# Kernel tuning notes

Hardware: AMD Instinct MI355X
Metric: run time of the kernel (lower is better)

The kernel has to match this reference:

```python
import jax, jax.numpy as jnp
import numpy as np

NUM_HEADS = 16
NEG_INF = -1e30  # finite large negative; avoids NaN on fully-masked padded query rows


def setup_inputs() -> dict:
    key = jax.random.key(0)
    k0, k1, k2, k3 = jax.random.split(key, 4)
    B, S, E = 4, 2048, 1024
    x_padded = jax.random.normal(k0, (B, S, E), dtype=jnp.float32)
    # variable lengths in [S//2, S] so no batch row is fully empty
    seq_lengths = jax.random.randint(k1, (B,), S // 2, S + 1).astype(jnp.int32)
    Wqkv = jax.random.normal(k2, (3 * E, E), dtype=jnp.float32) * 0.02  # torch Linear weight [out,in]
    Wout = jax.random.normal(k3, (E, E), dtype=jnp.float32) * 0.02
    return {"x_padded": x_padded, "Wqkv": Wqkv, "Wout": Wout,
            "seq_lengths": seq_lengths, "window_left": 512, "window_right": 0}


def _build_mask(seq_lengths, S, window_left, window_right):
    # key-side padding mask: [B, S]
    pad = jnp.arange(S)[None, :] < seq_lengths[:, None]
    mask = pad[:, None, None, :]  # [B,1,1,S]
    if window_left >= 0 or window_right >= 0:
        i = jnp.arange(S)[:, None]
        j = jnp.arange(S)[None, :]
        win = jnp.ones((S, S), dtype=bool)
        if window_left >= 0:
            win = win & (j >= i - window_left)
        if window_right >= 0:
            win = win & (j <= i + window_right)
        mask = mask & win[None, None, :, :]
    elif (window_left, window_right) == (-1, 0):
        causal = jnp.tril(jnp.ones((S, S), dtype=bool))
        mask = mask & causal[None, None, :, :]
    return mask  # [B,1,S,S] (broadcasts over heads)


def reference(x_padded, Wqkv, Wout, seq_lengths, window_left, window_right):
    B, S, E = x_padded.shape
    H = NUM_HEADS
    D = E // H
    scale = 1.0 / jnp.sqrt(jnp.float32(D))
    qkv = x_padded @ Wqkv.T  # [B,S,3E]
    q, k, v = jnp.split(qkv, 3, axis=-1)
    q = q.reshape(B, S, H, D).transpose(0, 2, 1, 3)  # [B,H,S,D]
    k = k.reshape(B, S, H, D).transpose(0, 2, 1, 3)
    v = v.reshape(B, S, H, D).transpose(0, 2, 1, 3)
    mask = _build_mask(seq_lengths, S, window_left, window_right)
    scores = jnp.einsum("bhid,bhjd->bhij", q, k) * scale
    scores = jnp.where(mask, scores, NEG_INF)
    attn = jax.nn.softmax(scores, axis=-1)
    out = jnp.einsum("bhij,bhjd->bhid", attn, v)  # [B,H,S,D]
    out = out.transpose(0, 2, 1, 3).reshape(B, S, E)
    return out @ Wout.T
```

## Files before the change

### kernel.cpp

```cpp
#include <hip/hip_runtime.h>

typedef __bf16 bf16;
typedef __attribute__((ext_vector_type(2))) __bf16 bf16x2;
typedef __attribute__((ext_vector_type(4))) __bf16 bf16x4;
typedef __attribute__((ext_vector_type(8))) __bf16 bf16x8;
typedef __attribute__((ext_vector_type(4))) float f32x4;
typedef __attribute__((ext_vector_type(16))) float f32x16;

#define B_ 4
#define S_ 2048
#define H_ 16
#define D_ 64
#define E_ 1024

#define BM 256
#define BN 128
#define BK 64

__device__ __forceinline__ int imin(int a, int b) { return a < b ? a : b; }
__device__ __forceinline__ int imax(int a, int b) { return a > b ? a : b; }

__device__ __forceinline__ void gload_lds16(const void* g, void* l) {
  __builtin_amdgcn_global_load_lds(
      (const __attribute__((address_space(1))) void*)g,
      (__attribute__((address_space(3))) void*)l, 16, 0, 0);
}

__global__ __launch_bounds__(256) void cvt3_kernel(
    const float* __restrict__ x, bf16* __restrict__ xb,
    const float* __restrict__ wqkv, bf16* __restrict__ wqkvb,
    const float* __restrict__ wout, bf16* __restrict__ woutb) {
  const int bid = blockIdx.x;
  const float* in;
  bf16* out;
  int idx;
  if (bid < 4096) { in = x; out = xb; idx = bid; }
  else if (bid < 5632) { in = wqkv; out = wqkvb; idx = bid - 4096; }
  else { in = wout; out = woutb; idx = bid - 5632; }
  const int i = (idx * 256 + threadIdx.x) * 8;
  float4 v0 = *(const float4*)(in + i);
  float4 v1 = *(const float4*)(in + i + 4);
  bf16x8 o;
  o[0] = (bf16)v0.x; o[1] = (bf16)v0.y; o[2] = (bf16)v0.z; o[3] = (bf16)v0.w;
  o[4] = (bf16)v1.x; o[5] = (bf16)v1.y; o[6] = (bf16)v1.z; o[7] = (bf16)v1.w;
  *(bf16x8*)(out + i) = o;
}

__global__ __launch_bounds__(512, 1) void gemm_pipe(
    const bf16* __restrict__ A, const bf16* __restrict__ Bm,
    int M, int N, int K, int mode,
    bf16* __restrict__ qd, bf16* __restrict__ kd, bf16* __restrict__ vtd,
    float* __restrict__ outf) {
  __shared__ __align__(16) bf16 As[3][BM * BK];
  __shared__ __align__(16) bf16 Bs[3][BN * BK];
  const int tid = threadIdx.x;
  const int wave = tid >> 6, lane = tid & 63;
  const int l15 = lane & 15, l4 = lane >> 4;
  const int wm = (wave >> 1) * 64;
  const int wn = (wave & 1) * 64;

  const int nwg = gridDim.x * gridDim.y;
  const int fid = blockIdx.y * gridDim.x + blockIdx.x;
  const int chunk = nwg >> 3;
  const int swz = (fid & 7) * chunk + (fid >> 3);
  const int tn = swz % gridDim.x;
  const int tm = swz / gridDim.x;

  const bf16* Abase = A + (size_t)tm * BM * K;
  const bf16* Bbase = Bm + (size_t)tn * BN * K;

  f32x4 acc[4][4];
#pragma unroll
  for (int i = 0; i < 4; ++i)
#pragma unroll
    for (int j = 0; j < 4; ++j)
#pragma unroll
      for (int r = 0; r < 4; ++r) acc[i][j][r] = 0.f;

  const int NT = K >> 6;

#define STAGE_A(sbuf, k0)                                                      \
  {                                                                            \
    _Pragma("unroll") for (int ld = 0; ld < 4; ++ld) {                         \
      const int idx = ld * 512 + tid;                                          \
      const int row = idx >> 3, g = idx & 7;                                   \
      const int gs = g ^ (row & 7);                                            \
      gload_lds16(Abase + (size_t)row * K + (k0) + gs * 8,                     \
                  As[sbuf] + (ld * 512 + wave * 64) * 8);                      \
    }                                                                          \
  }
#define STAGE_B(sbuf, k0)                                                      \
  {                                                                            \
    _Pragma("unroll") for (int ld = 0; ld < 2; ++ld) {                         \
      const int idx = ld * 512 + tid;                                          \
      const int row = idx >> 3, g = idx & 7;                                   \
      const int gs = g ^ (row & 7);                                            \
      gload_lds16(Bbase + (size_t)row * K + (k0) + gs * 8,                     \
                  Bs[sbuf] + (ld * 512 + wave * 64) * 8);                      \
    }                                                                          \
  }

  STAGE_A(0, 0); STAGE_B(0, 0);
  STAGE_A(1, BK); STAGE_B(1, BK);
  asm volatile("s_waitcnt vmcnt(6)" ::: "memory");
  __builtin_amdgcn_s_barrier();

  int p = 0;
  for (int t = 0; t < NT; ++t) {
    const bf16* Ap = As[p];
    const bf16* Bp = Bs[p];
    const int sb = (p + 2 >= 3) ? p - 1 : p + 2;
    const int sk0 = ((t + 2 < NT) ? t + 2 : NT - 1) * BK;

    bf16x8 a[4], bfr[4];
#pragma unroll
    for (int i = 0; i < 4; ++i) {
      const int ra = wm + i * 16 + l15;
      a[i] = *(const bf16x8*)(Ap + ra * 64 + ((l4 ^ (ra & 7)) * 8));
      const int rb = wn + i * 16 + l15;
      bfr[i] = *(const bf16x8*)(Bp + rb * 64 + ((l4 ^ (rb & 7)) * 8));
    }
    STAGE_A(sb, sk0);
    __builtin_amdgcn_s_barrier();
    asm volatile("s_waitcnt lgkmcnt(0)" ::: "memory");
    __builtin_amdgcn_sched_barrier(0);
    __builtin_amdgcn_s_setprio(1);
#pragma unroll
    for (int i = 0; i < 4; ++i)
#pragma unroll
      for (int j = 0; j < 4; ++j)
        acc[i][j] = __builtin_amdgcn_mfma_f32_16x16x32_bf16(a[i], bfr[j],
                                                            acc[i][j], 0, 0, 0);
    __builtin_amdgcn_s_setprio(0);
    __builtin_amdgcn_s_barrier();

#pragma unroll
    for (int i = 0; i < 4; ++i) {
      const int ra = wm + i * 16 + l15;
      a[i] = *(const bf16x8*)(Ap + ra * 64 + (((4 + l4) ^ (ra & 7)) * 8));
      const int rb = wn + i * 16 + l15;
      bfr[i] = *(const bf16x8*)(Bp + rb * 64 + (((4 + l4) ^ (rb & 7)) * 8));
    }
    STAGE_B(sb, sk0);
    __builtin_amdgcn_s_barrier();
    asm volatile("s_waitcnt lgkmcnt(0)" ::: "memory");
    __builtin_amdgcn_sched_barrier(0);
    __builtin_amdgcn_s_setprio(1);
#pragma unroll
    for (int i = 0; i < 4; ++i)
#pragma unroll
      for (int j = 0; j < 4; ++j)
        acc[i][j] = __builtin_amdgcn_mfma_f32_16x16x32_bf16(a[i], bfr[j],
                                                            acc[i][j], 0, 0, 0);
    __builtin_amdgcn_s_setprio(0);

    asm volatile("s_waitcnt vmcnt(6)" ::: "memory");
    __builtin_amdgcn_s_barrier();
    p = (p + 1 >= 3) ? 0 : p + 1;
  }
#undef STAGE_A
#undef STAGE_B

  if (mode == 0) {
#pragma unroll
    for (int i = 0; i < 4; ++i) {
      const int m0 = tm * BM + wm + i * 16 + l4 * 4;
      const int b = m0 >> 11, s = m0 & (S_ - 1);
#pragma unroll
      for (int j = 0; j < 4; ++j) {
        const int n = tn * BN + wn + j * 16 + l15;
        const int which = n >> 10;
        const int hn = n & 1023;
        const int h = hn >> 6, d = hn & 63;
        const f32x4 av = acc[i][j];
        if (which == 0) {
#pragma unroll
          for (int r = 0; r < 4; ++r)
            qd[((size_t)(b * H_ + h) * S_ + (s + r)) * D_ + d] =
                (bf16)(av[r] * 0.125f);
        } else if (which == 1) {
#pragma unroll
          for (int r = 0; r < 4; ++r)
            kd[((size_t)(b * H_ + h) * S_ + (s + r)) * D_ + d] = (bf16)av[r];
        } else {
          bf16x4 pv;
#pragma unroll
          for (int r = 0; r < 4; ++r) pv[r] = (bf16)av[r];
          *(bf16x4*)(vtd + ((size_t)(b * H_ + h) * D_ + d) * S_ + s) = pv;
        }
      }
    }
  } else {
#pragma unroll
    for (int i = 0; i < 4; ++i) {
      const int m0 = tm * BM + wm + i * 16 + l4 * 4;
#pragma unroll
      for (int j = 0; j < 4; ++j) {
        const int n = tn * BN + wn + j * 16 + l15;
#pragma unroll
        for (int r = 0; r < 4; ++r) outf[(size_t)(m0 + r) * N + n] = acc[i][j][r];
      }
    }
  }
}

__global__ __launch_bounds__(256) void meanv_kernel(const bf16* __restrict__ vt,
                                                    float* __restrict__ meanv) {
  const int bh = blockIdx.x >> 2, dq = blockIdx.x & 3;
  const int tid = threadIdx.x;
  const int dl = tid >> 4;
  const int sl = tid & 15;
  const int d = dq * 16 + dl;
  const bf16* row = vt + ((size_t)bh * D_ + d) * S_;
  float s = 0.f;
#pragma unroll
  for (int it = 0; it < 16; ++it) {
    bf16x8 v = *(const bf16x8*)(row + it * 128 + sl * 8);
#pragma unroll
    for (int j = 0; j < 8; ++j) s += (float)v[j];
  }
#pragma unroll
  for (int m = 1; m < 16; m <<= 1) s += __shfl_xor(s, m, 64);
  if (sl == 0) meanv[(size_t)bh * D_ + d] = s * (1.0f / (float)S_);
}

__device__ __forceinline__ int pk2(float a, float b) {
  union { bf16x2 h; int i; } u;
  u.h[0] = (bf16)a; u.h[1] = (bf16)b;
  return u.i;
}

__global__ __launch_bounds__(256) void attn_kernel(
    const bf16* __restrict__ q, const bf16* __restrict__ k,
    const bf16* __restrict__ vt, const float* __restrict__ meanv,
    const int* __restrict__ seq_lengths, const int* __restrict__ wlp,
    const int* __restrict__ wrp, bf16* __restrict__ attn_out) {
  __shared__ __align__(16) bf16 Ks[2][64 * 64];
  __shared__ __align__(16) bf16 Vs[2][64 * 64];
  const int tid = threadIdx.x, wave = tid >> 6, lane = tid & 63;
  const int l31 = lane & 31, l5 = lane >> 5;
  const int bid0 = blockIdx.x;
  const int bid = (bid0 & 7) * 128 + (bid0 >> 3);
  const int bh = bid >> 4;
  const int g = bid & 15;
  const int b = bh >> 4, h = bh & 15;
  const int q0b = g * 128;
  const int q0w = q0b + wave * 32;
  const int seq_len = seq_lengths[b];
  const int wl = wlp[0], wr = wrp[0];

  const bf16* qbase = q + (size_t)bh * S_ * D_;
  const bf16* kbase = k + (size_t)bh * S_ * D_;
  const bf16* vtb = vt + (size_t)bh * D_ * S_;

  bf16x8 qa[4];
#pragma unroll
  for (int dg = 0; dg < 4; ++dg)
    qa[dg] = *(const bf16x8*)(qbase + (size_t)(q0w + l31) * D_ + dg * 16 + l5 * 8);

  const int hi_blk = (wr >= 0) ? imin(q0b + 127 + wr, S_ - 1) : (S_ - 1);
  const int end_blk = imin(hi_blk + 1, seq_len);
  const int lo_blk = (wl >= 0) ? imax(0, q0b - wl) : 0;
  const int beg_blk = lo_blk & ~63;
  const int ntb = (end_blk > beg_blk) ? ((end_blk - beg_blk + 63) >> 6) : 0;

  const int w_hi = (wr >= 0) ? (q0w + 31 + wr) : (S_ - 1);
  const int w_end = imin(w_hi + 1, seq_len);
  const int w_lo = (wl >= 0) ? imax(0, q0w - wl) : 0;

  f32x16 o0, o1;
#pragma unroll
  for (int r = 0; r < 16; ++r) { o0[r] = 0.f; o1[r] = 0.f; }
  float mrun = -1e30f, lrun = 0.f;

#define STAGE(bufb, kt0)                                                       \
  {                                                                            \
    _Pragma("unroll") for (int ld = 0; ld < 2; ++ld) {                         \
      const int idx = ld * 256 + tid;                                          \
      const int row = idx >> 3, gg = idx & 7;                                  \
      const int gs = gg ^ (row & 7);                                           \
      const int krow = imin((kt0) + row, S_ - 1);                              \
      gload_lds16(kbase + (size_t)krow * 64 + gs * 8, Ks[bufb] + idx * 8);     \
      const int vcol = imin((kt0) + gs * 8, S_ - 8);                           \
      gload_lds16(vtb + (size_t)row * S_ + vcol, Vs[bufb] + idx * 8);          \
    }                                                                          \
  }
#define LDS_K(bufb, row, gran)                                                 \
  (*(const bf16x8*)((const char*)(Ks[bufb]) + (row) * 128 +                    \
                    (((gran) ^ ((row) & 7)) << 4)))
#define LDS_V(bufb, row, gran)                                                 \
  (*(const bf16x8*)((const char*)(Vs[bufb]) + (row) * 128 +                    \
                    (((gran) ^ ((row) & 7)) << 4)))

  if (ntb > 0) STAGE(0, beg_blk);
  __syncthreads();

  for (int t = 0; t < ntb; ++t) {
    const int kt = beg_blk + t * 64;
    if (t + 1 < ntb) STAGE((t + 1) & 1, kt + 64);

    const bool active = (kt < w_end) && (kt + 63 >= w_lo);
    if (active) {
      const int bufb = t & 1;
      f32x16 sf0, sf1;
#pragma unroll
      for (int r = 0; r < 16; ++r) { sf0[r] = 0.f; sf1[r] = 0.f; }
#pragma unroll
      for (int dg = 0; dg < 4; ++dg) {
        bf16x8 kb0 = LDS_K(bufb, l31, dg * 2 + l5);
        bf16x8 kb1 = LDS_K(bufb, 32 + l31, dg * 2 + l5);
        sf0 = __builtin_amdgcn_mfma_f32_32x32x16_bf16(kb0, qa[dg], sf0, 0, 0, 0);
        sf1 = __builtin_amdgcn_mfma_f32_32x32x16_bf16(kb1, qa[dg], sf1, 0, 0, 0);
      }

      bool allv = (kt + 63 < seq_len);
      if (wr >= 0) allv = allv && (kt + 63 <= q0w + wr);
      if (wl >= 0) allv = allv && (kt >= q0w + 31 - wl);
      if (!allv) {
        const int qrow = q0w + l31;
#pragma unroll
        for (int hh = 0; hh < 2; ++hh)
#pragma unroll
          for (int r = 0; r < 16; ++r) {
            const int key = kt + hh * 32 + (r & 3) + 8 * (r >> 2) + 4 * l5;
            bool valid = (key < seq_len);
            if (wr >= 0) valid = valid && (key <= qrow + wr);
            if (wl >= 0) valid = valid && (key >= qrow - wl);
            if (hh == 0) sf0[r] = valid ? sf0[r] : -1e30f;
            else sf1[r] = valid ? sf1[r] : -1e30f;
          }
      }
      float tmax = -1e30f;
#pragma unroll
      for (int r = 0; r < 16; ++r) {
        tmax = fmaxf(tmax, sf0[r]);
        tmax = fmaxf(tmax, sf1[r]);
      }
      tmax = fmaxf(tmax, __shfl_xor(tmax, 32, 64));

      if (!__all(tmax <= mrun + 8.0f)) {
        const float mnew = fmaxf(mrun, tmax);
        const float corr = __expf(mrun - mnew);
        mrun = mnew;
        lrun *= corr;
#pragma unroll
        for (int r = 0; r < 16; ++r) { o0[r] *= corr; o1[r] *= corr; }
      }

      float lsum = 0.f;
#pragma unroll
      for (int r = 0; r < 16; ++r) {
        const float e0 = (sf0[r] <= -1e29f) ? 0.f : __expf(sf0[r] - mrun);
        const float e1 = (sf1[r] <= -1e29f) ? 0.f : __expf(sf1[r] - mrun);
        sf0[r] = e0; sf1[r] = e1;
        lsum += e0 + e1;
      }
      lsum += __shfl_xor(lsum, 32, 64);
      lrun += lsum;

      bf16x8 pb[4];
#pragma unroll
      for (int kg = 0; kg < 4; ++kg) {
        const int base = (kg & 1) * 8;
        float p0, p1, p2, p3, p4, p5, p6, p7;
        if (kg < 2) {
          p0 = sf0[base + 0]; p1 = sf0[base + 1]; p2 = sf0[base + 2];
          p3 = sf0[base + 3]; p4 = sf0[base + 4]; p5 = sf0[base + 5];
          p6 = sf0[base + 6]; p7 = sf0[base + 7];
        } else {
          p0 = sf1[base + 0]; p1 = sf1[base + 1]; p2 = sf1[base + 2];
          p3 = sf1[base + 3]; p4 = sf1[base + 4]; p5 = sf1[base + 5];
          p6 = sf1[base + 6]; p7 = sf1[base + 7];
        }
        const int w0 = pk2(p0, p1);
        const int w1 = pk2(p2, p3);
        const int w2 = pk2(p4, p5);
        const int w3 = pk2(p6, p7);
        auto r02 = __builtin_amdgcn_permlane32_swap(w0, w2, false, false);
        auto r13 = __builtin_amdgcn_permlane32_swap(w1, w3, false, false);
        union { int i[4]; bf16x8 v; } u;
        u.i[0] = r02[0]; u.i[1] = r13[0]; u.i[2] = r02[1]; u.i[3] = r13[1];
        pb[kg] = u.v;
      }

#pragma unroll
      for (int kg = 0; kg < 4; ++kg) {
        bf16x8 va0 = LDS_V(bufb, l31, kg * 2 + l5);
        bf16x8 va1 = LDS_V(bufb, 32 + l31, kg * 2 + l5);
        o0 = __builtin_amdgcn_mfma_f32_32x32x16_bf16(va0, pb[kg], o0, 0, 0, 0);
        o1 = __builtin_amdgcn_mfma_f32_32x32x16_bf16(va1, pb[kg], o1, 0, 0, 0);
      }
    }
    __syncthreads();
  }
#undef STAGE
#undef LDS_K
#undef LDS_V

  const int qrow = q0w + l31;
  bf16* outp = attn_out + ((size_t)(b * S_ + qrow)) * E_ + h * 64;
  if (lrun > 0.f) {
    const float inv = 1.0f / lrun;
#pragma unroll
    for (int dg2 = 0; dg2 < 2; ++dg2) {
      const f32x16& o = dg2 ? o1 : o0;
#pragma unroll
      for (int rg = 0; rg < 4; ++rg) {
        const int d0 = dg2 * 32 + 8 * rg + 4 * l5;
        bf16x4 ov;
#pragma unroll
        for (int j = 0; j < 4; ++j) ov[j] = (bf16)(o[rg * 4 + j] * inv);
        *(bf16x4*)(outp + d0) = ov;
      }
    }
  } else {
    const float* mv = meanv + (size_t)bh * D_;
#pragma unroll
    for (int dg2 = 0; dg2 < 2; ++dg2)
#pragma unroll
      for (int rg = 0; rg < 4; ++rg) {
        const int d0 = dg2 * 32 + 8 * rg + 4 * l5;
        bf16x4 ov;
#pragma unroll
        for (int j = 0; j < 4; ++j) ov[j] = (bf16)mv[d0 + j];
        *(bf16x4*)(outp + d0) = ov;
      }
  }
}

extern "C" void kernel_launch(void* const* d_in, const int* in_sizes, int n_in,
                              void* d_out, int out_size, void* d_ws, size_t ws_size,
                              hipStream_t stream) {
  const float* x = (const float*)d_in[0];
  const float* Wqkv = (const float*)d_in[1];
  const float* Wout = (const float*)d_in[2];
  const int* seq_lengths = (const int*)d_in[3];
  const int* wl = (const int*)d_in[4];
  const int* wr = (const int*)d_in[5];
  float* out = (float*)d_out;

  char* ws = (char*)d_ws;
  bf16* xb = (bf16*)ws;      ws += (size_t)8192 * 1024 * 2;
  bf16* wqkvb = (bf16*)ws;   ws += (size_t)3072 * 1024 * 2;
  bf16* woutb = (bf16*)ws;   ws += (size_t)1024 * 1024 * 2;
  bf16* qd = (bf16*)ws;      ws += (size_t)B_ * H_ * S_ * D_ * 2;
  bf16* kd = (bf16*)ws;      ws += (size_t)B_ * H_ * S_ * D_ * 2;
  bf16* vtd = (bf16*)ws;     ws += (size_t)B_ * H_ * S_ * D_ * 2;
  bf16* attn = (bf16*)ws;    ws += (size_t)8192 * 1024 * 2;
  float* meanv = (float*)ws; ws += (size_t)B_ * H_ * D_ * 4;

  cvt3_kernel<<<6144, 256, 0, stream>>>(x, xb, Wqkv, wqkvb, Wout, woutb);

  gemm_pipe<<<dim3(24, 32), 512, 0, stream>>>(xb, wqkvb, 8192, 3072, 1024, 0,
                                              qd, kd, vtd, nullptr);
  meanv_kernel<<<256, 256, 0, stream>>>(vtd, meanv);
  attn_kernel<<<1024, 256, 0, stream>>>(qd, kd, vtd, meanv, seq_lengths, wl, wr,
                                        attn);
  gemm_pipe<<<dim3(8, 32), 512, 0, stream>>>(attn, woutb, 8192, 1024, 1024, 1,
                                             nullptr, nullptr, nullptr, out);
}
```

Before: 179.6 us.

## Switch projection GEMMs to 256x256 tiles with double-buffered interleaved staging

Replaces the 256x128 triple-buffered GEMM with a 256x256 tile kernel using 8 waves, each computing 128x64, and a double-buffered pipeline that splits each K step into four MFMA sub-phases with global-to-LDS loads interleaved. The goal is higher arithmetic intensity and less global/LDS traffic per output. In exchange it halves the number of workgroups, which underfills the CUs for the output projection, and it waits for all outstanding loads each step.

Result: slower. 187.5 us (+4.4%).

```diff
diff --git a/kernel.cpp b/kernel.cpp
--- a/kernel.cpp
+++ b/kernel.cpp
@@ -12,10 +12,6 @@
 #define H_ 16
 #define D_ 64
 #define E_ 1024
-
-#define BM 256
-#define BN 128
-#define BK 64
 
 __device__ __forceinline__ int imin(int a, int b) { return a < b ? a : b; }
 __device__ __forceinline__ int imax(int a, int b) { return a > b ? a : b; }
@@ -46,18 +42,18 @@
   *(bf16x8*)(out + i) = o;
 }
 
-__global__ __launch_bounds__(512, 1) void gemm_pipe(
+__global__ __launch_bounds__(512, 1) void gemm8(
     const bf16* __restrict__ A, const bf16* __restrict__ Bm,
-    int M, int N, int K, int mode,
+    int K, int mode, int N,
     bf16* __restrict__ qd, bf16* __restrict__ kd, bf16* __restrict__ vtd,
     float* __restrict__ outf) {
-  __shared__ __align__(16) bf16 As[3][BM * BK];
-  __shared__ __align__(16) bf16 Bs[3][BN * BK];
+  __shared__ __align__(16) bf16 As[2][256 * 64];
+  __shared__ __align__(16) bf16 Bs[2][256 * 64];
   const int tid = threadIdx.x;
   const int wave = tid >> 6, lane = tid & 63;
   const int l15 = lane & 15, l4 = lane >> 4;
-  const int wm = (wave >> 1) * 64;
-  const int wn = (wave & 1) * 64;
+  const int wm = (wave >> 2) * 128;
+  const int wn = (wave & 3) * 64;
 
   const int nwg = gridDim.x * gridDim.y;
   const int fid = blockIdx.y * gridDim.x + blockIdx.x;
@@ -66,141 +62,181 @@
   const int tn = swz % gridDim.x;
   const int tm = swz / gridDim.x;
 
-  const bf16* Abase = A + (size_t)tm * BM * K;
-  const bf16* Bbase = Bm + (size_t)tn * BN * K;
-
-  f32x4 acc[4][4];
-#pragma unroll
-  for (int i = 0; i < 4; ++i)
+  const bf16* Abase = A + (size_t)tm * 256 * K;
+  const bf16* Bbase = Bm + (size_t)tn * 256 * K;
+
+  f32x4 acc[8][4];
+#pragma unroll
+  for (int i = 0; i < 8; ++i)
 #pragma unroll
     for (int j = 0; j < 4; ++j)
 #pragma unroll
       for (int r = 0; r < 4; ++r) acc[i][j][r] = 0.f;
 
   const int NT = K >> 6;
-
-#define STAGE_A(sbuf, k0)                                                      \
-  {                                                                            \
-    _Pragma("unroll") for (int ld = 0; ld < 4; ++ld) {                         \
-      const int idx = ld * 512 + tid;                                          \
-      const int row = idx >> 3, g = idx & 7;                                   \
-      const int gs = g ^ (row & 7);                                            \
-      gload_lds16(Abase + (size_t)row * K + (k0) + gs * 8,                     \
-                  As[sbuf] + (ld * 512 + wave * 64) * 8);                      \
-    }                                                                          \
-  }
-#define STAGE_B(sbuf, k0)                                                      \
+  const int NI = K >> 7;
+
+#define STG8(lds, gb, half, k0)                                                \
   {                                                                            \
     _Pragma("unroll") for (int ld = 0; ld < 2; ++ld) {                         \
       const int idx = ld * 512 + tid;                                          \
-      const int row = idx >> 3, g = idx & 7;                                   \
-      const int gs = g ^ (row & 7);                                            \
-      gload_lds16(Bbase + (size_t)row * K + (k0) + gs * 8,                     \
-                  Bs[sbuf] + (ld * 512 + wave * 64) * 8);                      \
+      const int row = (half) * 128 + (idx >> 3);                               \
+      const int gs = (idx & 7) ^ (row & 7);                                    \
+      gload_lds16((gb) + (size_t)row * K + (k0) + gs * 8,                      \
+                  (lds) + (half) * 8192 + idx * 8);                            \
     }                                                                          \
   }
-
-  STAGE_A(0, 0); STAGE_B(0, 0);
-  STAGE_A(1, BK); STAGE_B(1, BK);
-  asm volatile("s_waitcnt vmcnt(6)" ::: "memory");
+#define RD(ldsbuf, r, ks)                                                      \
+  (*(const bf16x8*)((ldsbuf) + (r) * 64 + ((((ks) * 4 + l4) ^ ((r) & 7)) * 8)))
+
+  STG8(As[0], Abase, 0, 0); STG8(As[0], Abase, 1, 0);
+  STG8(Bs[0], Bbase, 0, 0); STG8(Bs[0], Bbase, 1, 0);
+  asm volatile("s_waitcnt vmcnt(0)" ::: "memory");
   __builtin_amdgcn_s_barrier();
 
-  int p = 0;
-  for (int t = 0; t < NT; ++t) {
-    const bf16* Ap = As[p];
-    const bf16* Bp = Bs[p];
-    const int sb = (p + 2 >= 3) ? p - 1 : p + 2;
-    const int sk0 = ((t + 2 < NT) ? t + 2 : NT - 1) * BK;
-
-    bf16x8 a[4], bfr[4];
-#pragma unroll
-    for (int i = 0; i < 4; ++i) {
-      const int ra = wm + i * 16 + l15;
-      a[i] = *(const bf16x8*)(Ap + ra * 64 + ((l4 ^ (ra & 7)) * 8));
-      const int rb = wn + i * 16 + l15;
-      bfr[i] = *(const bf16x8*)(Bp + rb * 64 + ((l4 ^ (rb & 7)) * 8));
+  bf16x8 af[4][2], bfv[4][2];
+
+  for (int it = 0; it < NI; ++it) {
+    const int kA = (2 * it + 1) << 6;
+    const int t2 = 2 * it + 2;
+    const int kB = ((t2 < NT) ? t2 : NT - 1) << 6;
+
+#pragma unroll
+    for (int half = 0; half < 2; ++half) {
+      const bf16* Ap = As[half];
+      const bf16* Bp = Bs[half];
+      bf16* Asd = As[half ^ 1];
+      bf16* Bsd = Bs[half ^ 1];
+      const int kS = half ? kB : kA;
+
+#pragma unroll
+      for (int i = 0; i < 4; ++i) {
+        const int ra = wm + i * 16 + l15;
+        af[i][0] = RD(Ap, ra, 0);
+        af[i][1] = RD(Ap, ra, 1);
+      }
+#pragma unroll
+      for (int c = 0; c < 4; ++c) {
+        const int rb = wn + (c >> 1) * 32 + (c & 1) * 16 + l15;
+        bfv[c][0] = RD(Bp, rb, 0);
+        bfv[c][1] = RD(Bp, rb, 1);
+      }
+      STG8(Asd, Abase, 0, kS);
+      __builtin_amdgcn_s_barrier();
+      asm volatile("s_waitcnt lgkmcnt(0)" ::: "memory");
+      __builtin_amdgcn_sched_barrier(0);
+      __builtin_amdgcn_s_setprio(1);
+#pragma unroll
+      for (int ks = 0; ks < 2; ++ks)
+#pragma unroll
+        for (int i = 0; i < 4; ++i)
+#pragma unroll
+          for (int j = 0; j < 2; ++j)
+            acc[i][j] = __builtin_amdgcn_mfma_f32_16x16x32_bf16(
+                af[i][ks], bfv[j][ks], acc[i][j], 0, 0, 0);
+      __builtin_amdgcn_s_setprio(0);
+      __builtin_amdgcn_s_barrier();
+
+      STG8(Asd, Abase, 1, kS);
+      __builtin_amdgcn_s_barrier();
+      __builtin_amdgcn_s_setprio(1);
+#pragma unroll
+      for (int ks = 0; ks < 2; ++ks)
+#pragma unroll
+        for (int i = 0; i < 4; ++i)
+#pragma unroll
+          for (int j = 0; j < 2; ++j)
+            acc[i][2 + j] = __builtin_amdgcn_mfma_f32_16x16x32_bf16(
+                af[i][ks], bfv[2 + j][ks], acc[i][2 + j], 0, 0, 0);
+      __builtin_amdgcn_s_setprio(0);
+      __builtin_amdgcn_s_barrier();
+
+#pragma unroll
+      for (int i = 0; i < 4; ++i) {
+        const int ra = wm + 64 + i * 16 + l15;
+        af[i][0] = RD(Ap, ra, 0);
+        af[i][1] = RD(Ap, ra, 1);
+      }
+      STG8(Bsd, Bbase, 0, kS);
+      __builtin_amdgcn_s_barrier();
+      asm volatile("s_waitcnt lgkmcnt(0)" ::: "memory");
+      __builtin_amdgcn_sched_barrier(0);
+      __builtin_amdgcn_s_setprio(1);
+#pragma unroll
+      for (int ks = 0; ks < 2; ++ks)
+#pragma unroll
+        for (int i = 0; i < 4; ++i)
+#pragma unroll
+          for (int j = 0; j < 2; ++j)
+            acc[4 + i][j] = __builtin_amdgcn_mfma_f32_16x16x32_bf16(
+                af[i][ks], bfv[j][ks], acc[4 + i][j], 0, 0, 0);
+      __builtin_amdgcn_s_setprio(0);
+      __builtin_amdgcn_s_barrier();
+
+      STG8(Bsd, Bbase, 1, kS);
+      __builtin_amdgcn_s_barrier();
+      __builtin_amdgcn_s_setprio(1);
+#pragma unroll
+      for (int ks = 0; ks < 2; ++ks)
+#pragma unroll
+        for (int i = 0; i < 4; ++i)
+#pragma unroll
+          for (int j = 0; j < 2; ++j)
+            acc[4 + i][2 + j] = __builtin_amdgcn_mfma_f32_16x16x32_bf16(
+                af[i][ks], bfv[2 + j][ks], acc[4 + i][2 + j], 0, 0, 0);
+      __builtin_amdgcn_s_setprio(0);
+      asm volatile("s_waitcnt vmcnt(0)" ::: "memory");
+      __builtin_amdgcn_s_barrier();
     }
-    STAGE_A(sb, sk0);
-    __builtin_amdgcn_s_barrier();
-    asm volatile("s_waitcnt lgkmcnt(0)" ::: "memory");
-    __builtin_amdgcn_sched_barrier(0);
-    __builtin_amdgcn_s_setprio(1);
-#pragma unroll
-    for (int i = 0; i < 4; ++i)
-#pragma unroll
-      for (int j = 0; j < 4; ++j)
-        acc[i][j] = __builtin_amdgcn_mfma_f32_16x16x32_bf16(a[i], bfr[j],
-                                                            acc[i][j], 0, 0, 0);
-    __builtin_amdgcn_s_setprio(0);
-    __builtin_amdgcn_s_barrier();
-
-#pragma unroll
-    for (int i = 0; i < 4; ++i) {
-      const int ra = wm + i * 16 + l15;
-      a[i] = *(const bf16x8*)(Ap + ra * 64 + (((4 + l4) ^ (ra & 7)) * 8));
-      const int rb = wn + i * 16 + l15;
-      bfr[i] = *(const bf16x8*)(Bp + rb * 64 + (((4 + l4) ^ (rb & 7)) * 8));
-    }
-    STAGE_B(sb, sk0);
-    __builtin_amdgcn_s_barrier();
-    asm volatile("s_waitcnt lgkmcnt(0)" ::: "memory");
-    __builtin_amdgcn_sched_barrier(0);
-    __builtin_amdgcn_s_setprio(1);
-#pragma unroll
-    for (int i = 0; i < 4; ++i)
-#pragma unroll
-      for (int j = 0; j < 4; ++j)
-        acc[i][j] = __builtin_amdgcn_mfma_f32_16x16x32_bf16(a[i], bfr[j],
-                                                            acc[i][j], 0, 0, 0);
-    __builtin_amdgcn_s_setprio(0);
-
-    asm volatile("s_waitcnt vmcnt(6)" ::: "memory");
-    __builtin_amdgcn_s_barrier();
-    p = (p + 1 >= 3) ? 0 : p + 1;
-  }
-#undef STAGE_A
-#undef STAGE_B
+  }
+#undef STG8
+#undef RD
 
   if (mode == 0) {
 #pragma unroll
-    for (int i = 0; i < 4; ++i) {
-      const int m0 = tm * BM + wm + i * 16 + l4 * 4;
-      const int b = m0 >> 11, s = m0 & (S_ - 1);
-#pragma unroll
-      for (int j = 0; j < 4; ++j) {
-        const int n = tn * BN + wn + j * 16 + l15;
-        const int which = n >> 10;
-        const int hn = n & 1023;
-        const int h = hn >> 6, d = hn & 63;
-        const f32x4 av = acc[i][j];
-        if (which == 0) {
+    for (int ms = 0; ms < 2; ++ms)
+#pragma unroll
+      for (int mi = 0; mi < 4; ++mi) {
+        const int m0 = tm * 256 + wm + ms * 64 + mi * 16 + l4 * 4;
+        const int b = m0 >> 11, s = m0 & (S_ - 1);
+#pragma unroll
+        for (int nc = 0; nc < 4; ++nc) {
+          const int n = tn * 256 + wn + (nc >> 1) * 32 + (nc & 1) * 16 + l15;
+          const int which = n >> 10;
+          const int hn = n & 1023;
+          const int h = hn >> 6, d = hn & 63;
+          const f32x4 av = acc[ms * 4 + mi][nc];
+          if (which == 0) {
+#pragma unroll
+            for (int r = 0; r < 4; ++r)
+              qd[((size_t)(b * H_ + h) * S_ + (s + r)) * D_ + d] =
+                  (bf16)(av[r] * 0.125f);
+          } else if (which == 1) {
+#pragma unroll
+            for (int r = 0; r < 4; ++r)
+              kd[((size_t)(b * H_ + h) * S_ + (s + r)) * D_ + d] = (bf16)av[r];
+          } else {
+            bf16x4 pv;
+#pragma unroll
+            for (int r = 0; r < 4; ++r) pv[r] = (bf16)av[r];
+            *(bf16x4*)(vtd + ((size_t)(b * H_ + h) * D_ + d) * S_ + s) = pv;
+          }
+        }
+      }
+  } else {
+#pragma unroll
+    for (int ms = 0; ms < 2; ++ms)
+#pragma unroll
+      for (int mi = 0; mi < 4; ++mi) {
+        const int m0 = tm * 256 + wm + ms * 64 + mi * 16 + l4 * 4;
+#pragma unroll
+        for (int nc = 0; nc < 4; ++nc) {
+          const int n = tn * 256 + wn + (nc >> 1) * 32 + (nc & 1) * 16 + l15;
 #pragma unroll
           for (int r = 0; r < 4; ++r)
-            qd[((size_t)(b * H_ + h) * S_ + (s + r)) * D_ + d] =
-                (bf16)(av[r] * 0.125f);
-        } else if (which == 1) {
-#pragma unroll
-          for (int r = 0; r < 4; ++r)
-            kd[((size_t)(b * H_ + h) * S_ + (s + r)) * D_ + d] = (bf16)av[r];
-        } else {
-          bf16x4 pv;
-#pragma unroll
-          for (int r = 0; r < 4; ++r) pv[r] = (bf16)av[r];
-          *(bf16x4*)(vtd + ((size_t)(b * H_ + h) * D_ + d) * S_ + s) = pv;
+            outf[(size_t)(m0 + r) * N + n] = acc[ms * 4 + mi][nc][r];
         }
       }
-    }
-  } else {
-#pragma unroll
-    for (int i = 0; i < 4; ++i) {
-      const int m0 = tm * BM + wm + i * 16 + l4 * 4;
-#pragma unroll
-      for (int j = 0; j < 4; ++j) {
-        const int n = tn * BN + wn + j * 16 + l15;
-#pragma unroll
-        for (int r = 0; r < 4; ++r) outf[(size_t)(m0 + r) * N + n] = acc[i][j][r];
-      }
-    }
   }
 }
 
@@ -451,11 +487,11 @@
 
   cvt3_kernel<<<6144, 256, 0, stream>>>(x, xb, Wqkv, wqkvb, Wout, woutb);
 
-  gemm_pipe<<<dim3(24, 32), 512, 0, stream>>>(xb, wqkvb, 8192, 3072, 1024, 0,
-                                              qd, kd, vtd, nullptr);
+  gemm8<<<dim3(12, 32), 512, 0, stream>>>(xb, wqkvb, 1024, 0, 3072,
+                                          qd, kd, vtd, nullptr);
   meanv_kernel<<<256, 256, 0, stream>>>(vtd, meanv);
   attn_kernel<<<1024, 256, 0, stream>>>(qd, kd, vtd, meanv, seq_lengths, wl, wr,
                                         attn);
-  gemm_pipe<<<dim3(8, 32), 512, 0, stream>>>(attn, woutb, 8192, 1024, 1024, 1,
-                                             nullptr, nullptr, nullptr, out);
-}
+  gemm8<<<dim3(4, 32), 512, 0, stream>>>(attn, woutb, 1024, 1, 1024,
+                                         nullptr, nullptr, nullptr, out);
+}
```

## Double query rows per attention wave and drop mid-iteration GEMM barriers

Applied to the files above, without the earlier changes.

The attention kernel now gives each wave 64 query rows as two 32-row halves instead of 32, and each block 256 rows instead of 128, halving the grid. Each K/V tile staged in LDS and each K/V fragment read into registers is therefore reused across twice as many queries. Separately, the GEMM main loop drops the intermediate s_barrier, lgkmcnt waits and sched_barriers around the MFMA phases. This relies on the compiler's own waitcnt insertion and risks losing the intended wave interleaving. Larger per-wave accumulators raise register pressure, and the windowed tiles per block span more keys, with fewer blocks to fill the CUs.

New measurement: 220.5 us. 1.23x slower.

```diff
diff --git a/kernel.cpp b/kernel.cpp
--- a/kernel.cpp
+++ b/kernel.cpp
@@ -121,9 +121,6 @@
       bfr[i] = *(const bf16x8*)(Bp + rb * 64 + ((l4 ^ (rb & 7)) * 8));
     }
     STAGE_A(sb, sk0);
-    __builtin_amdgcn_s_barrier();
-    asm volatile("s_waitcnt lgkmcnt(0)" ::: "memory");
-    __builtin_amdgcn_sched_barrier(0);
     __builtin_amdgcn_s_setprio(1);
 #pragma unroll
     for (int i = 0; i < 4; ++i)
@@ -132,8 +129,6 @@
         acc[i][j] = __builtin_amdgcn_mfma_f32_16x16x32_bf16(a[i], bfr[j],
                                                             acc[i][j], 0, 0, 0);
     __builtin_amdgcn_s_setprio(0);
-    __builtin_amdgcn_s_barrier();
-
 #pragma unroll
     for (int i = 0; i < 4; ++i) {
       const int ra = wm + i * 16 + l15;
@@ -142,9 +137,6 @@
       bfr[i] = *(const bf16x8*)(Bp + rb * 64 + (((4 + l4) ^ (rb & 7)) * 8));
     }
     STAGE_B(sb, sk0);
-    __builtin_amdgcn_s_barrier();
-    asm volatile("s_waitcnt lgkmcnt(0)" ::: "memory");
-    __builtin_amdgcn_sched_barrier(0);
     __builtin_amdgcn_s_setprio(1);
 #pragma unroll
     for (int i = 0; i < 4; ++i)
@@ -240,12 +232,12 @@
   const int tid = threadIdx.x, wave = tid >> 6, lane = tid & 63;
   const int l31 = lane & 31, l5 = lane >> 5;
   const int bid0 = blockIdx.x;
-  const int bid = (bid0 & 7) * 128 + (bid0 >> 3);
-  const int bh = bid >> 4;
-  const int g = bid & 15;
+  const int bid = (bid0 & 7) * 64 + (bid0 >> 3);
+  const int bh = bid >> 3;
+  const int g = bid & 7;
   const int b = bh >> 4, h = bh & 15;
-  const int q0b = g * 128;
-  const int q0w = q0b + wave * 32;
+  const int q0b = g * 256;
+  const int q0w = q0b + wave * 64;
   const int seq_len = seq_lengths[b];
   const int wl = wlp[0], wr = wrp[0];
 
@@ -253,25 +245,32 @@
   const bf16* kbase = k + (size_t)bh * S_ * D_;
   const bf16* vtb = vt + (size_t)bh * D_ * S_;
 
-  bf16x8 qa[4];
-#pragma unroll
-  for (int dg = 0; dg < 4; ++dg)
-    qa[dg] = *(const bf16x8*)(qbase + (size_t)(q0w + l31) * D_ + dg * 16 + l5 * 8);
-
-  const int hi_blk = (wr >= 0) ? imin(q0b + 127 + wr, S_ - 1) : (S_ - 1);
+  bf16x8 qa[2][4];
+#pragma unroll
+  for (int h2 = 0; h2 < 2; ++h2)
+#pragma unroll
+    for (int dg = 0; dg < 4; ++dg)
+      qa[h2][dg] = *(const bf16x8*)(qbase + (size_t)(q0w + h2 * 32 + l31) * D_ +
+                                    dg * 16 + l5 * 8);
+
+  const int hi_blk = (wr >= 0) ? imin(q0b + 255 + wr, S_ - 1) : (S_ - 1);
   const int end_blk = imin(hi_blk + 1, seq_len);
   const int lo_blk = (wl >= 0) ? imax(0, q0b - wl) : 0;
   const int beg_blk = lo_blk & ~63;
   const int ntb = (end_blk > beg_blk) ? ((end_blk - beg_blk + 63) >> 6) : 0;
 
-  const int w_hi = (wr >= 0) ? (q0w + 31 + wr) : (S_ - 1);
+  const int w_hi = (wr >= 0) ? (q0w + 63 + wr) : (S_ - 1);
   const int w_end = imin(w_hi + 1, seq_len);
   const int w_lo = (wl >= 0) ? imax(0, q0w - wl) : 0;
 
-  f32x16 o0, o1;
-#pragma unroll
-  for (int r = 0; r < 16; ++r) { o0[r] = 0.f; o1[r] = 0.f; }
-  float mrun = -1e30f, lrun = 0.f;
+  f32x16 o[2][2];
+#pragma unroll
+  for (int h2 = 0; h2 < 2; ++h2)
+#pragma unroll
+    for (int dv = 0; dv < 2; ++dv)
+#pragma unroll
+      for (int r = 0; r < 16; ++r) o[h2][dv][r] = 0.f;
+  float mrun[2] = {-1e30f, -1e30f}, lrun[2] = {0.f, 0.f};
 
 #define STAGE(bufb, kt0)                                                       \
   {                                                                            \
@@ -302,93 +301,110 @@
     const bool active = (kt < w_end) && (kt + 63 >= w_lo);
     if (active) {
       const int bufb = t & 1;
-      f32x16 sf0, sf1;
-#pragma unroll
-      for (int r = 0; r < 16; ++r) { sf0[r] = 0.f; sf1[r] = 0.f; }
+      bf16x8 kf0[4], kf1[4];
 #pragma unroll
       for (int dg = 0; dg < 4; ++dg) {
-        bf16x8 kb0 = LDS_K(bufb, l31, dg * 2 + l5);
-        bf16x8 kb1 = LDS_K(bufb, 32 + l31, dg * 2 + l5);
-        sf0 = __builtin_amdgcn_mfma_f32_32x32x16_bf16(kb0, qa[dg], sf0, 0, 0, 0);
-        sf1 = __builtin_amdgcn_mfma_f32_32x32x16_bf16(kb1, qa[dg], sf1, 0, 0, 0);
+        kf0[dg] = LDS_K(bufb, l31, dg * 2 + l5);
+        kf1[dg] = LDS_K(bufb, 32 + l31, dg * 2 + l5);
       }
-
-      bool allv = (kt + 63 < seq_len);
-      if (wr >= 0) allv = allv && (kt + 63 <= q0w + wr);
-      if (wl >= 0) allv = allv && (kt >= q0w + 31 - wl);
-      if (!allv) {
-        const int qrow = q0w + l31;
-#pragma unroll
-        for (int hh = 0; hh < 2; ++hh)
+      f32x16 sf[2][2];
+#pragma unroll
+      for (int h2 = 0; h2 < 2; ++h2)
+#pragma unroll
+        for (int kv = 0; kv < 2; ++kv)
+#pragma unroll
+          for (int r = 0; r < 16; ++r) sf[h2][kv][r] = 0.f;
+#pragma unroll
+      for (int h2 = 0; h2 < 2; ++h2)
+#pragma unroll
+        for (int dg = 0; dg < 4; ++dg) {
+          sf[h2][0] = __builtin_amdgcn_mfma_f32_32x32x16_bf16(
+              kf0[dg], qa[h2][dg], sf[h2][0], 0, 0, 0);
+          sf[h2][1] = __builtin_amdgcn_mfma_f32_32x32x16_bf16(
+              kf1[dg], qa[h2][dg], sf[h2][1], 0, 0, 0);
+        }
+
+      bf16x8 pb[2][4];
+#pragma unroll
+      for (int h2 = 0; h2 < 2; ++h2) {
+        const int qlo = q0w + h2 * 32;
+        bool allv = (kt + 63 < seq_len);
+        if (wr >= 0) allv = allv && (kt + 63 <= qlo + wr);
+        if (wl >= 0) allv = allv && (kt >= qlo + 31 - wl);
+        if (!allv) {
+          const int qrow = qlo + l31;
+#pragma unroll
+          for (int kv = 0; kv < 2; ++kv)
+#pragma unroll
+            for (int r = 0; r < 16; ++r) {
+              const int key = kt + kv * 32 + (r & 3) + 8 * (r >> 2) + 4 * l5;
+              bool valid = (key < seq_len);
+              if (wr >= 0) valid = valid && (key <= qrow + wr);
+              if (wl >= 0) valid = valid && (key >= qrow - wl);
+              sf[h2][kv][r] = valid ? sf[h2][kv][r] : -1e30f;
+            }
+        }
+        float tmax = -1e30f;
+#pragma unroll
+        for (int r = 0; r < 16; ++r) {
+          tmax = fmaxf(tmax, sf[h2][0][r]);
+          tmax = fmaxf(tmax, sf[h2][1][r]);
+        }
+        tmax = fmaxf(tmax, __shfl_xor(tmax, 32, 64));
+
+        if (!__all(tmax <= mrun[h2] + 8.0f)) {
+          const float mnew = fmaxf(mrun[h2], tmax);
+          const float corr = __expf(mrun[h2] - mnew);
+          mrun[h2] = mnew;
+          lrun[h2] *= corr;
 #pragma unroll
           for (int r = 0; r < 16; ++r) {
-            const int key = kt + hh * 32 + (r & 3) + 8 * (r >> 2) + 4 * l5;
-            bool valid = (key < seq_len);
-            if (wr >= 0) valid = valid && (key <= qrow + wr);
-            if (wl >= 0) valid = valid && (key >= qrow - wl);
-            if (hh == 0) sf0[r] = valid ? sf0[r] : -1e30f;
-            else sf1[r] = valid ? sf1[r] : -1e30f;
+            o[h2][0][r] *= corr;
+            o[h2][1][r] *= corr;
           }
-      }
-      float tmax = -1e30f;
-#pragma unroll
-      for (int r = 0; r < 16; ++r) {
-        tmax = fmaxf(tmax, sf0[r]);
-        tmax = fmaxf(tmax, sf1[r]);
-      }
-      tmax = fmaxf(tmax, __shfl_xor(tmax, 32, 64));
-
-      if (!__all(tmax <= mrun + 8.0f)) {
-        const float mnew = fmaxf(mrun, tmax);
-        const float corr = __expf(mrun - mnew);
-        mrun = mnew;
-        lrun *= corr;
-#pragma unroll
-        for (int r = 0; r < 16; ++r) { o0[r] *= corr; o1[r] *= corr; }
-      }
-
-      float lsum = 0.f;
-#pragma unroll
-      for (int r = 0; r < 16; ++r) {
-        const float e0 = (sf0[r] <= -1e29f) ? 0.f : __expf(sf0[r] - mrun);
-        const float e1 = (sf1[r] <= -1e29f) ? 0.f : __expf(sf1[r] - mrun);
-        sf0[r] = e0; sf1[r] = e1;
-        lsum += e0 + e1;
-      }
-      lsum += __shfl_xor(lsum, 32, 64);
-      lrun += lsum;
-
-      bf16x8 pb[4];
-#pragma unroll
-      for (int kg = 0; kg < 4; ++kg) {
-        const int base = (kg & 1) * 8;
-        float p0, p1, p2, p3, p4, p5, p6, p7;
-        if (kg < 2) {
-          p0 = sf0[base + 0]; p1 = sf0[base + 1]; p2 = sf0[base + 2];
-          p3 = sf0[base + 3]; p4 = sf0[base + 4]; p5 = sf0[base + 5];
-          p6 = sf0[base + 6]; p7 = sf0[base + 7];
-        } else {
-          p0 = sf1[base + 0]; p1 = sf1[base + 1]; p2 = sf1[base + 2];
-          p3 = sf1[base + 3]; p4 = sf1[base + 4]; p5 = sf1[base + 5];
-          p6 = sf1[base + 6]; p7 = sf1[base + 7];
-        }
-        const int w0 = pk2(p0, p1);
-        const int w1 = pk2(p2, p3);
-        const int w2 = pk2(p4, p5);
-        const int w3 = pk2(p6, p7);
-        auto r02 = __builtin_amdgcn_permlane32_swap(w0, w2, false, false);
-        auto r13 = __builtin_amdgcn_permlane32_swap(w1, w3, false, false);
-        union { int i[4]; bf16x8 v; } u;
-        u.i[0] = r02[0]; u.i[1] = r13[0]; u.i[2] = r02[1]; u.i[3] = r13[1];
-        pb[kg] = u.v;
+        }
+
+        float lsum = 0.f;
+#pragma unroll
+        for (int kv = 0; kv < 2; ++kv)
+#pragma unroll
+          for (int r = 0; r < 16; ++r) {
+            const float e = (sf[h2][kv][r] <= -1e29f)
+                                ? 0.f
+                                : __expf(sf[h2][kv][r] - mrun[h2]);
+            sf[h2][kv][r] = e;
+            lsum += e;
+          }
+        lsum += __shfl_xor(lsum, 32, 64);
+        lrun[h2] += lsum;
+
+#pragma unroll
+        for (int kg = 0; kg < 4; ++kg) {
+          const int kv = kg >> 1;
+          const int base = (kg & 1) * 8;
+          const int w0 = pk2(sf[h2][kv][base + 0], sf[h2][kv][base + 1]);
+          const int w1 = pk2(sf[h2][kv][base + 2], sf[h2][kv][base + 3]);
+          const int w2 = pk2(sf[h2][kv][base + 4], sf[h2][kv][base + 5]);
+          const int w3 = pk2(sf[h2][kv][base + 6], sf[h2][kv][base + 7]);
+          auto r02 = __builtin_amdgcn_permlane32_swap(w0, w2, false, false);
+          auto r13 = __builtin_amdgcn_permlane32_swap(w1, w3, false, false);
+          union { int i[4]; bf16x8 v; } u;
+          u.i[0] = r02[0]; u.i[1] = r13[0]; u.i[2] = r02[1]; u.i[3] = r13[1];
+          pb[h2][kg] = u.v;
+        }
       }
 
 #pragma unroll
       for (int kg = 0; kg < 4; ++kg) {
         bf16x8 va0 = LDS_V(bufb, l31, kg * 2 + l5);
         bf16x8 va1 = LDS_V(bufb, 32 + l31, kg * 2 + l5);
-        o0 = __builtin_amdgcn_mfma_f32_32x32x16_bf16(va0, pb[kg], o0, 0, 0, 0);
-        o1 = __builtin_amdgcn_mfma_f32_32x32x16_bf16(va1, pb[kg], o1, 0, 0, 0);
+#pragma unroll
+        for (int h2 = 0; h2 < 2; ++h2) {
+          o[h2][0] = __builtin_amdgcn_mfma_f32_32x32x16_bf16(va0, pb[h2][kg],
+                                                             o[h2][0], 0, 0, 0);
+          o[h2][1] = __builtin_amdgcn_mfma_f32_32x32x16_bf16(va1, pb[h2][kg],
+                                                             o[h2][1], 0, 0, 0);
+        }
       }
     }
     __syncthreads();
@@ -397,34 +413,35 @@
 #undef LDS_K
 #undef LDS_V
 
-  const int qrow = q0w + l31;
-  bf16* outp = attn_out + ((size_t)(b * S_ + qrow)) * E_ + h * 64;
-  if (lrun > 0.f) {
-    const float inv = 1.0f / lrun;
-#pragma unroll
-    for (int dg2 = 0; dg2 < 2; ++dg2) {
-      const f32x16& o = dg2 ? o1 : o0;
-#pragma unroll
-      for (int rg = 0; rg < 4; ++rg) {
-        const int d0 = dg2 * 32 + 8 * rg + 4 * l5;
-        bf16x4 ov;
-#pragma unroll
-        for (int j = 0; j < 4; ++j) ov[j] = (bf16)(o[rg * 4 + j] * inv);
-        *(bf16x4*)(outp + d0) = ov;
-      }
-    }
-  } else {
-    const float* mv = meanv + (size_t)bh * D_;
-#pragma unroll
-    for (int dg2 = 0; dg2 < 2; ++dg2)
-#pragma unroll
-      for (int rg = 0; rg < 4; ++rg) {
-        const int d0 = dg2 * 32 + 8 * rg + 4 * l5;
-        bf16x4 ov;
-#pragma unroll
-        for (int j = 0; j < 4; ++j) ov[j] = (bf16)mv[d0 + j];
-        *(bf16x4*)(outp + d0) = ov;
-      }
+#pragma unroll
+  for (int h2 = 0; h2 < 2; ++h2) {
+    const int qrow = q0w + h2 * 32 + l31;
+    bf16* outp = attn_out + ((size_t)(b * S_ + qrow)) * E_ + h * 64;
+    if (lrun[h2] > 0.f) {
+      const float inv = 1.0f / lrun[h2];
+#pragma unroll
+      for (int dv = 0; dv < 2; ++dv)
+#pragma unroll
+        for (int rg = 0; rg < 4; ++rg) {
+          const int d0 = dv * 32 + 8 * rg + 4 * l5;
+          bf16x4 ov;
+#pragma unroll
+          for (int j = 0; j < 4; ++j) ov[j] = (bf16)(o[h2][dv][rg * 4 + j] * inv);
+          *(bf16x4*)(outp + d0) = ov;
+        }
+    } else {
+      const float* mv = meanv + (size_t)bh * D_;
+#pragma unroll
+      for (int dv = 0; dv < 2; ++dv)
+#pragma unroll
+        for (int rg = 0; rg < 4; ++rg) {
+          const int d0 = dv * 32 + 8 * rg + 4 * l5;
+          bf16x4 ov;
+#pragma unroll
+          for (int j = 0; j < 4; ++j) ov[j] = (bf16)mv[d0 + j];
+          *(bf16x4*)(outp + d0) = ov;
+        }
+    }
   }
 }
 
@@ -454,8 +471,8 @@
   gemm_pipe<<<dim3(24, 32), 512, 0, stream>>>(xb, wqkvb, 8192, 3072, 1024, 0,
                                               qd, kd, vtd, nullptr);
   meanv_kernel<<<256, 256, 0, stream>>>(vtd, meanv);
-  attn_kernel<<<1024, 256, 0, stream>>>(qd, kd, vtd, meanv, seq_lengths, wl, wr,
-                                        attn);
+  attn_kernel<<<512, 256, 0, stream>>>(qd, kd, vtd, meanv, seq_lengths, wl, wr,
+                                       attn);
   gemm_pipe<<<dim3(8, 32), 512, 0, stream>>>(attn, woutb, 8192, 1024, 1024, 1,
                                              nullptr, nullptr, nullptr, out);
 }
```
